# Kernel optimization log

Hardware: AMD Instinct MI355X
Metric: run time of the kernel (lower is better)

## Reference

```python
import jax, jax.numpy as jnp
import numpy as np

B, V, F, HO = 4096, 64, 128, 3  # batch, num_variable (agents), num_factor, highest_orders


def setup_inputs() -> dict:
    key = jax.random.key(0)
    logits = jax.random.normal(key, (B, V, F), dtype=jnp.float32)
    # softmax is normalized over the variable axis (dim=1), per factor
    softmax = jax.nn.softmax(logits, axis=1)
    log_probs = jax.nn.log_softmax(logits, axis=1)
    return {"softmax": softmax, "log_probs": log_probs}


def reference(softmax, log_probs):
    # softmax, log_probs: [B, V, F]
    softmax_pre = jnp.transpose(softmax, (0, 2, 1))  # [B, F, V]
    # deterministic (explore=False) path: top-k over variables per factor
    value, indices = jax.lax.top_k(softmax_pre, HO)  # [B, F, 3], descending (matches torch.topk largest)
    v0, v1, v2 = value[..., 0], value[..., 1], value[..., 2]
    p_order3 = v0 ** 3
    p_order2 = 3.0 * v1 * v2 * (v1 + v2)
    p_order1 = 6.0 * v0 * v1 * v2
    chosen_order3 = (p_order3 > p_order2) & (p_order3 > p_order1)
    chosen_order2 = (p_order2 >= p_order3) & (p_order2 > p_order1)  # disjoint from order3
    i0 = indices[..., 0]
    i1 = jnp.where(chosen_order3, i0, indices[..., 1])
    i2 = jnp.where(chosen_order3 | chosen_order2, i0, indices[..., 2])
    indices = jnp.stack([i0, i1, i2], axis=-1)  # [B, F, 3]

    # entropy per (variable, factor), summed over variables, mean over factors
    entropy = -(softmax * log_probs)
    ent = entropy.sum(-2).mean(-1)  # [B]

    cond_adj_1 = (softmax > 0.01).astype(jnp.int32)  # [B, V, F]
    # scatter 1s at selected variable indices along V, per (batch, factor)
    bi = jnp.arange(B)[:, None, None]
    fi = jnp.arange(F)[None, :, None]
    cond_adj_2 = jnp.zeros((B, F, V), jnp.int32).at[bi, fi, indices].set(1)
    cond_adj_2 = jnp.transpose(cond_adj_2, (0, 2, 1))  # [B, V, F]
    cond_adj = cond_adj_1 & cond_adj_2
    return softmax, cond_adj, ent
```

## Files before the change

### kernel.cpp

```cpp
#include <hip/hip_runtime.h>

constexpr int Bn  = 4096;
constexpr int Vn  = 64;
constexpr int Fn  = 128;
constexpr int NPB = Vn * Fn;

typedef float f32x4 __attribute__((ext_vector_type(4)));
typedef unsigned long long u64;

__device__ __forceinline__ void kins(u64 k, u64& m0, u64& m1, u64& m2) {
    const u64 a = m0 > k ? m0 : k;
    const u64 b = m0 > k ? k  : m0;
    m0 = a;
    const u64 c = m1 > b ? m1 : b;
    const u64 d = m1 > b ? b  : m1;
    m1 = c;
    m2 = m2 > d ? m2 : d;
}

__global__ __launch_bounds__(256)
void adj_generator_kernel(const float* __restrict__ sm_g,
                          float* __restrict__ out_sm,
                          float* __restrict__ out_adj,
                          float* __restrict__ out_ent) {
    const int wv = threadIdx.x >> 6;
    const int l  = threadIdx.x & 63;
    const int b  = blockIdx.x * 4 + wv;

    const f32x4* s4 = (const f32x4*)(sm_g   + (size_t)b * NPB);
    f32x4*       o4 = (f32x4*)(out_sm + (size_t)b * NPB);

    u64 m0[4], m1[4], m2[4];
    #pragma unroll
    for (int c = 0; c < 4; ++c) { m0[c] = 0; m1[c] = 0; m2[c] = 0; }

    unsigned int pr[4] = {0u, 0u, 0u, 0u};
    float esum = 0.0f;
    const int rbase = l >> 5;

    #pragma unroll 8
    for (int i = 0; i < 32; ++i) {
        const int idx = l + 64 * i;
        const f32x4 v = __builtin_nontemporal_load(&s4[idx]);
        __builtin_nontemporal_store(v, &o4[idx]);
        esum -= v.x * __logf(v.x) + v.y * __logf(v.y)
              + v.z * __logf(v.z) + v.w * __logf(v.w);
        pr[0] |= (v.x > 0.01f ? 1u : 0u) << i;
        pr[1] |= (v.y > 0.01f ? 1u : 0u) << i;
        pr[2] |= (v.z > 0.01f ? 1u : 0u) << i;
        pr[3] |= (v.w > 0.01f ? 1u : 0u) << i;
        const u64 rk = (u64)(63 ^ (rbase + 2 * i));
        kins(((u64)__float_as_uint(v.x) << 6) | rk, m0[0], m1[0], m2[0]);
        kins(((u64)__float_as_uint(v.y) << 6) | rk, m0[1], m1[1], m2[1]);
        kins(((u64)__float_as_uint(v.z) << 6) | rk, m0[2], m1[2], m2[2]);
        kins(((u64)__float_as_uint(v.w) << 6) | rk, m0[3], m1[3], m2[3]);
    }

    #pragma unroll
    for (int c = 0; c < 4; ++c) {
        const u64 p0 = (u64)__shfl_xor((long long)m0[c], 32);
        const u64 p1 = (u64)__shfl_xor((long long)m1[c], 32);
        const u64 p2 = (u64)__shfl_xor((long long)m2[c], 32);
        kins(p0, m0[c], m1[c], m2[c]);
        kins(p1, m0[c], m1[c], m2[c]);
        kins(p2, m0[c], m1[c], m2[c]);
    }

    #pragma unroll
    for (int off = 32; off > 0; off >>= 1)
        esum += __shfl_down(esum, off);
    if (l == 0)
        out_ent[b] = esum * (1.0f / Fn);

    u64 q[4];
    #pragma unroll
    for (int c = 0; c < 4; ++c) {
        const float v0 = __uint_as_float((unsigned)(m0[c] >> 6));
        const float v1 = __uint_as_float((unsigned)(m1[c] >> 6));
        const float v2 = __uint_as_float((unsigned)(m2[c] >> 6));
        const int   i0 = 63 ^ (int)(m0[c] & 63);
        const int   i1 = 63 ^ (int)(m1[c] & 63);
        const int   i2 = 63 ^ (int)(m2[c] & 63);
        const float p3  = __fmul_rn(__fmul_rn(v0, v0), v0);
        const float p2_ = __fmul_rn(__fmul_rn(__fmul_rn(3.0f, v1), v2), __fadd_rn(v1, v2));
        const float p1_ = __fmul_rn(__fmul_rn(__fmul_rn(6.0f, v0), v1), v2);
        const bool c3 = (p3  > p2_) && (p3  > p1_);
        const bool c2 = (p2_ >= p3) && (p2_ > p1_);
        const int  j1 = c3 ? i0 : i1;
        const int  j2 = (c3 || c2) ? i0 : i2;
        q[c] = (1ull << i0) | (1ull << j1) | (1ull << j2);
    }

    f32x4* a4 = (f32x4*)(out_adj + (size_t)b * NPB);
    #pragma unroll 8
    for (int i = 0; i < 32; ++i) {
        const int idx = l + 64 * i;
        const int r   = rbase + 2 * i;
        f32x4 a;
        a.x = (((pr[0] >> i) & 1u) && ((q[0] >> r) & 1ull)) ? 1.0f : 0.0f;
        a.y = (((pr[1] >> i) & 1u) && ((q[1] >> r) & 1ull)) ? 1.0f : 0.0f;
        a.z = (((pr[2] >> i) & 1u) && ((q[2] >> r) & 1ull)) ? 1.0f : 0.0f;
        a.w = (((pr[3] >> i) & 1u) && ((q[3] >> r) & 1ull)) ? 1.0f : 0.0f;
        __builtin_nontemporal_store(a, &a4[idx]);
    }
}

extern "C" void kernel_launch(void* const* d_in, const int* in_sizes, int n_in,
                              void* d_out, int out_size, void* d_ws, size_t ws_size,
                              hipStream_t stream) {
    const float* softmax = (const float*)d_in[0];

    float* out     = (float*)d_out;
    float* out_sm  = out;
    float* out_adj = out + (size_t)Bn * NPB;
    float* out_ent = out + 2 * (size_t)Bn * NPB;

    adj_generator_kernel<<<Bn / 4, 256, 0, stream>>>(softmax, out_sm, out_adj, out_ent);
}
```

Measured before the change: 79.57 us.

## Double-buffer input through LDS with async global_load_lds and manual vmcnt waits

```diff
diff --git a/kernel.cpp b/kernel.cpp
--- a/kernel.cpp
+++ b/kernel.cpp
@@ -7,6 +7,12 @@
 
 typedef float f32x4 __attribute__((ext_vector_type(4)));
 typedef unsigned long long u64;
+
+typedef const float __attribute__((address_space(1)))* gas1;
+typedef float __attribute__((address_space(3)))*       las3;
+
+#define WAITVM(n) asm volatile("s_waitcnt vmcnt(" #n ")" ::: "memory")
+#define CFENCE()  asm volatile("" ::: "memory")
 
 __device__ __forceinline__ void kins(u64 k, u64& m0, u64& m1, u64& m2) {
     const u64 a = m0 > k ? m0 : k;
@@ -23,38 +29,60 @@
                           float* __restrict__ out_sm,
                           float* __restrict__ out_adj,
                           float* __restrict__ out_ent) {
+    __shared__ f32x4 stage[4][2][512];
+
     const int wv = threadIdx.x >> 6;
     const int l  = threadIdx.x & 63;
     const int b  = blockIdx.x * 4 + wv;
 
-    const f32x4* s4 = (const f32x4*)(sm_g   + (size_t)b * NPB);
-    f32x4*       o4 = (f32x4*)(out_sm + (size_t)b * NPB);
+    const float* gsrc = sm_g + (size_t)b * NPB;
+    f32x4* o4 = (f32x4*)(out_sm  + (size_t)b * NPB);
+    f32x4* a4 = (f32x4*)(out_adj + (size_t)b * NPB);
 
     u64 m0[4], m1[4], m2[4];
     #pragma unroll
     for (int c = 0; c < 4; ++c) { m0[c] = 0; m1[c] = 0; m2[c] = 0; }
-
-    unsigned int pr[4] = {0u, 0u, 0u, 0u};
+    unsigned pr[4] = {0u, 0u, 0u, 0u};
     float esum = 0.0f;
     const int rbase = l >> 5;
 
-    #pragma unroll 8
-    for (int i = 0; i < 32; ++i) {
-        const int idx = l + 64 * i;
-        const f32x4 v = __builtin_nontemporal_load(&s4[idx]);
-        __builtin_nontemporal_store(v, &o4[idx]);
-        esum -= v.x * __logf(v.x) + v.y * __logf(v.y)
-              + v.z * __logf(v.z) + v.w * __logf(v.w);
-        pr[0] |= (v.x > 0.01f ? 1u : 0u) << i;
-        pr[1] |= (v.y > 0.01f ? 1u : 0u) << i;
-        pr[2] |= (v.z > 0.01f ? 1u : 0u) << i;
-        pr[3] |= (v.w > 0.01f ? 1u : 0u) << i;
-        const u64 rk = (u64)(63 ^ (rbase + 2 * i));
-        kins(((u64)__float_as_uint(v.x) << 6) | rk, m0[0], m1[0], m2[0]);
-        kins(((u64)__float_as_uint(v.y) << 6) | rk, m0[1], m1[1], m2[1]);
-        kins(((u64)__float_as_uint(v.z) << 6) | rk, m0[2], m1[2], m2[2]);
-        kins(((u64)__float_as_uint(v.w) << 6) | rk, m0[3], m1[3], m2[3]);
-    }
+    auto stage_sc = [&](int buf, int sc) {
+        #pragma unroll
+        for (int c = 0; c < 8; ++c) {
+            const float* gp = gsrc + sc * 2048 + c * 256 + l * 4;
+            __builtin_amdgcn_global_load_lds((gas1)gp,
+                                             (las3)&stage[wv][buf][c * 64],
+                                             16, 0, 0);
+        }
+        CFENCE();
+    };
+
+    auto process = [&](int buf, int sc) {
+        #pragma unroll
+        for (int i = 0; i < 8; ++i) {
+            const int I = sc * 8 + i;
+            const f32x4 v = stage[wv][buf][i * 64 + l];
+            __builtin_nontemporal_store(v, &o4[l + 64 * I]);
+            esum -= v.x * __log2f(v.x) + v.y * __log2f(v.y)
+                  + v.z * __log2f(v.z) + v.w * __log2f(v.w);
+            pr[0] |= (v.x > 0.01f ? 1u : 0u) << I;
+            pr[1] |= (v.y > 0.01f ? 1u : 0u) << I;
+            pr[2] |= (v.z > 0.01f ? 1u : 0u) << I;
+            pr[3] |= (v.w > 0.01f ? 1u : 0u) << I;
+            const u64 rk = (u64)(63 ^ (rbase + 2 * I));
+            kins(((u64)__float_as_uint(v.x) << 6) | rk, m0[0], m1[0], m2[0]);
+            kins(((u64)__float_as_uint(v.y) << 6) | rk, m0[1], m1[1], m2[1]);
+            kins(((u64)__float_as_uint(v.z) << 6) | rk, m0[2], m1[2], m2[2]);
+            kins(((u64)__float_as_uint(v.w) << 6) | rk, m0[3], m1[3], m2[3]);
+        }
+        CFENCE();
+    };
+
+    stage_sc(0, 0);
+    stage_sc(1, 1); WAITVM(8);  process(0, 0);
+    stage_sc(0, 2); WAITVM(16); process(1, 1);
+    stage_sc(1, 3); WAITVM(16); process(0, 2);
+                    WAITVM(8);  process(1, 3);
 
     #pragma unroll
     for (int c = 0; c < 4; ++c) {
@@ -70,7 +98,7 @@
     for (int off = 32; off > 0; off >>= 1)
         esum += __shfl_down(esum, off);
     if (l == 0)
-        out_ent[b] = esum * (1.0f / Fn);
+        out_ent[b] = esum * (0.69314718055994530942f / 128.0f);
 
     u64 q[4];
     #pragma unroll
@@ -91,17 +119,15 @@
         q[c] = (1ull << i0) | (1ull << j1) | (1ull << j2);
     }
 
-    f32x4* a4 = (f32x4*)(out_adj + (size_t)b * NPB);
     #pragma unroll 8
-    for (int i = 0; i < 32; ++i) {
-        const int idx = l + 64 * i;
-        const int r   = rbase + 2 * i;
+    for (int I = 0; I < 32; ++I) {
+        const int r = rbase + 2 * I;
         f32x4 a;
-        a.x = (((pr[0] >> i) & 1u) && ((q[0] >> r) & 1ull)) ? 1.0f : 0.0f;
-        a.y = (((pr[1] >> i) & 1u) && ((q[1] >> r) & 1ull)) ? 1.0f : 0.0f;
-        a.z = (((pr[2] >> i) & 1u) && ((q[2] >> r) & 1ull)) ? 1.0f : 0.0f;
-        a.w = (((pr[3] >> i) & 1u) && ((q[3] >> r) & 1ull)) ? 1.0f : 0.0f;
-        __builtin_nontemporal_store(a, &a4[idx]);
+        a.x = (((pr[0] >> I) & 1u) && ((q[0] >> r) & 1ull)) ? 1.0f : 0.0f;
+        a.y = (((pr[1] >> I) & 1u) && ((q[1] >> r) & 1ull)) ? 1.0f : 0.0f;
+        a.z = (((pr[2] >> I) & 1u) && ((q[2] >> r) & 1ull)) ? 1.0f : 0.0f;
+        a.w = (((pr[3] >> I) & 1u) && ((q[3] >> r) & 1ull)) ? 1.0f : 0.0f;
+        __builtin_nontemporal_store(a, &a4[l + 64 * I]);
     }
 }
 
```

Result: faster. 63.92 us (-19.7%).
